# Optimization experiments

Measured on AMD Instinct MI355X. Metric: run time of the kernel, lower is better.

The kernel has to match this reference:

```python
import jax, jax.numpy as jnp
import numpy as np

WIN = 9
EPS = 1e-05


def _box3d(x, win=WIN):
    """Sum over a win^3 box (zero-padded), equivalent to conv3d with a ones kernel.
    Implemented as three separable 1D convolutions (exact same math, O(win)/voxel)."""
    pad = win // 2
    for axis in range(3):  # spatial axes D, H, W
        kshape = [1, 1, 1, 1, 1]
        kshape[2 + axis] = win
        kern = jnp.ones(kshape, x.dtype)
        pads = [(0, 0)] * 3
        pads[axis] = (pad, pad)
        dn = jax.lax.conv_dimension_numbers(x.shape, kern.shape, ('NCDHW', 'OIDHW', 'NCDHW'))
        x = jax.lax.conv_general_dilated(x, kern, window_strides=(1, 1, 1),
                                         padding=pads, dimension_numbers=dn)
    return x


def setup_inputs() -> dict:
    key = jax.random.key(0)
    k1, k2 = jax.random.split(key)
    shape = (1, 1, 160, 192, 224)  # [N, C, D, H, W] brain-MRI-scale volume
    I = jax.random.normal(k1, shape, dtype=jnp.float32)
    J = jax.random.normal(k2, shape, dtype=jnp.float32)
    return {"I": I, "J": J}


def reference(I, J):
    win_size = WIN ** 3
    I2 = I * I
    J2 = J * J
    IJ = I * J
    I_sum = _box3d(I)
    J_sum = _box3d(J)
    I2_sum = _box3d(I2)
    J2_sum = _box3d(J2)
    IJ_sum = _box3d(IJ)
    u_I = I_sum / win_size
    u_J = J_sum / win_size
    cross = IJ_sum - u_J * I_sum - u_I * J_sum + u_I * u_J * win_size
    I_var = I2_sum - 2 * u_I * I_sum + u_I * u_I * win_size
    J_var = J2_sum - 2 * u_J * J_sum + u_J * u_J * win_size
    cc = cross * cross / (I_var * J_var + EPS)
    return -1.0 * jnp.mean(cc)
```

## Files before the change

### kernel.cpp

```cpp
#include <hip/hip_runtime.h>


#define DD 160
#define HH 192
#define WW 224
#define W4 56
#define SLICE (HH * WW)
#define S4 (SLICE / 4)
#define NVOX (DD * SLICE)
#define TW 32
#define TH 8
#define DCH 28
#define ITERS (DCH + 8)
#define NTHR 256
#define SW_RS 36
#define SW_CS (16 * SW_RS)
#define SH_SZ (TH * TW * 5)
#define EPS 1e-5f
#define INV_WSUM (1.0f / 729.0f)

__device__ __forceinline__ void bar_lds_only() {
    __asm__ volatile("" ::: "memory");
    __builtin_amdgcn_s_waitcnt(0xC07F);
    __builtin_amdgcn_s_barrier();
    __asm__ volatile("" ::: "memory");
}

__global__ __launch_bounds__(NTHR, 4) void ncc_fused(const float* __restrict__ I,
                                                     const float* __restrict__ J,
                                                     float* __restrict__ out) {
    __shared__ float SW0[5 * SW_CS], SW1[5 * SW_CS];
    __shared__ float SH0[SH_SZ], SH1[SH_SZ];
    __shared__ float wred[NTHR / 64];

    const int tid = threadIdx.x;
    const int tx = tid & 31, ty = tid >> 5;
    const int wlo = blockIdx.x * TW;
    const int hlo = blockIdx.y * TH;
    const int dlo = blockIdx.z * DCH;

    const int wid = tid - 128;
    const int wr = wid >> 3, wc = wid & 7;
    const int gh = hlo - 4 + wr;
    const bool hok = (gh >= 0) && (gh < HH);
    const int gf0 = (wlo >> 2) - 1 + wc;

    const int hcol = tid & 31, hch = tid >> 5;

    const float4* Iv = (const float4*)I;
    const float4* Jv = (const float4*)J;

    float pfa[12], pfb[12];

    auto w_load = [&](int z) {
        const bool zok = (z >= 0) && (z < DD) && hok;
        const int rowb = z * S4 + gh * W4;
        #pragma unroll
        for (int k = 0; k < 3; ++k) {
            const int f = gf0 + k;
            float4 a = make_float4(0.f, 0.f, 0.f, 0.f);
            float4 b = make_float4(0.f, 0.f, 0.f, 0.f);
            if (zok && f >= 0 && f < W4) { a = Iv[rowb + f]; b = Jv[rowb + f]; }
            pfa[4*k] = a.x; pfa[4*k+1] = a.y; pfa[4*k+2] = a.z; pfa[4*k+3] = a.w;
            pfb[4*k] = b.x; pfb[4*k+1] = b.y; pfb[4*k+2] = b.z; pfb[4*k+3] = b.w;
        }
    };

    auto w_compute = [&](float* dst) {
        float* wp = dst + wr * SW_RS + 4 * wc;
        #pragma unroll
        for (int ch = 0; ch < 5; ++ch) {
            float v[12];
            #pragma unroll
            for (int k = 0; k < 12; ++k)
                v[k] = (ch == 0) ? pfa[k]
                     : (ch == 1) ? pfb[k]
                     : (ch == 2) ? pfa[k] * pfa[k]
                     : (ch == 3) ? pfb[k] * pfb[k]
                     :             pfa[k] * pfb[k];
            float s = v[0];
            #pragma unroll
            for (int k = 1; k < 9; ++k) s += v[k];
            float4 o;
            o.x = s;
            s += v[9]  - v[0]; o.y = s;
            s += v[10] - v[1]; o.z = s;
            s += v[11] - v[2]; o.w = s;
            *(float4*)(wp + ch * SW_CS) = o;
        }
    };

    auto h_phase = [&](const float* swSrc, float* shDst) {
        const float* p = swSrc + hch * SW_CS + hcol;
        float v[16];
        #pragma unroll
        for (int r = 0; r < 16; r += 2) {
            const float* pr = p + r * SW_RS;
            v[r]     = pr[0];
            v[r + 1] = pr[SW_RS];
        }
        float s = v[0];
        #pragma unroll
        for (int r = 1; r < 9; ++r) s += v[r];
        float* o = shDst + hcol * 5 + hch;
        float prev = s;
        o[0] = s;
        #pragma unroll
        for (int r = 1; r < TH; ++r) {
            prev += v[r + 8] - v[r - 1];
            o[r * (TW * 5)] = prev;
        }
    };

    float q0[9], q1[9], q2[9], q3[9], q4[9];
    #pragma unroll
    for (int k = 0; k < 9; ++k) { q0[k]=0.f; q1[k]=0.f; q2[k]=0.f; q3[k]=0.f; q4[k]=0.f; }
    float r0=0.f, r1=0.f, r2=0.f, r3=0.f, r4=0.f;
    float acc = 0.f;

    const int z0 = dlo - 4;
    if (tid >= 128) {
        w_load(z0);
        if (z0 >= 0) w_compute(SW0);
        w_load(z0 + 1);
    }
    bar_lds_only();

    if (tid < 160 && z0 >= 0) h_phase(SW0, SH0);
    if (tid >= 128) {
        const int z1 = z0 + 1;
        if (z1 >= 0 && z1 < DD) w_compute(SW1);
        w_load(z0 + 2);
    }

    #pragma unroll 1
    for (int g = 0; g < 4; ++g) {
        #pragma unroll
        for (int ph = 0; ph < 9; ++ph) {
            const int j = 9 * g + ph;
            const int z = dlo - 4 + j;
            bar_lds_only();

            const bool val = (z >= 0) && (z < DD);
            float* shR = (j & 1) ? SH1 : SH0;
            float w0=0.f, w1=0.f, w2=0.f, w3=0.f, w4=0.f;
            if (val) {
                const float* pF = shR + (ty * TW + tx) * 5;
                w0 = pF[0]; w1 = pF[1]; w2 = pF[2]; w3 = pF[3]; w4 = pF[4];
            }

            if ((g < 3 || ph < 8) && tid < 160) {
                const int zh = z + 1;
                if (zh >= 0 && zh < DD)
                    h_phase((j & 1) ? SW0 : SW1, (j & 1) ? SH0 : SH1);
            }

            if ((g < 3 || ph < 7) && tid >= 128) {
                const int zw = z + 2;
                if (zw >= 0 && zw < DD) w_compute((j & 1) ? SW1 : SW0);
                w_load(z + 3);
            }

            r0 += w0 - q0[ph]; q0[ph] = w0;
            r1 += w1 - q1[ph]; q1[ph] = w1;
            r2 += w2 - q2[ph]; q2[ph] = w2;
            r3 += w3 - q3[ph]; q3[ph] = w3;
            r4 += w4 - q4[ph]; q4[ph] = w4;

            if (j >= 8 && (dlo + j - 8) < DD) {
                float cross = r4 - r0 * r1 * INV_WSUM;
                float iv    = r2 - r0 * r0 * INV_WSUM;
                float jv    = r3 - r1 * r1 * INV_WSUM;
                acc += cross * cross * __builtin_amdgcn_rcpf(iv * jv + EPS);
            }
        }
    }

    #pragma unroll
    for (int off = 32; off > 0; off >>= 1) acc += __shfl_down(acc, off, 64);
    if ((tid & 63) == 0) wred[tid >> 6] = acc;
    __syncthreads();
    if (tid == 0) {
        float t = 0.f;
        #pragma unroll
        for (int k = 0; k < NTHR / 64; ++k) t += wred[k];
        atomicAdd(out, t * (-1.0f / (float)NVOX));
    }
}

extern "C" void kernel_launch(void* const* d_in, const int* in_sizes, int n_in,
                              void* d_out, int out_size, void* d_ws, size_t ws_size,
                              hipStream_t stream) {
    const float* I = (const float*)d_in[0];
    const float* J = (const float*)d_in[1];
    float* out = (float*)d_out;

    hipMemsetAsync(d_out, 0, sizeof(float), stream);

    dim3 blk(NTHR, 1, 1);
    dim3 grd(WW / TW, HH / TH, (DD + DCH - 1) / DCH);
    ncc_fused<<<grd, blk, 0, stream>>>(I, J, out);
}
```

Before: 126.0 us.

## Double-buffer global prefetch registers to load two depth slices ahead

Adds a second set of prefetch registers so global loads for slice z+4 are issued while slice z+2 is being processed, deepening the load pipeline from one slice ahead to two. The inner loop is unrolled to 18 phases so the register-buffer choice and the LDS-buffer parity stay compile-time constant, and the ring index becomes ph%9. This aims to hide more global-memory latency, at the cost of 24 extra VGPRs per thread and a larger unrolled body, which could lower occupancy under the 4-blocks-per-SM launch bound.

```diff
diff --git a/kernel.cpp b/kernel.cpp
--- a/kernel.cpp
+++ b/kernel.cpp
@@ -50,45 +50,51 @@
     const float4* Iv = (const float4*)I;
     const float4* Jv = (const float4*)J;
 
-    float pfa[12], pfb[12];
-
-    auto w_load = [&](int z) {
-        const bool zok = (z >= 0) && (z < DD) && hok;
-        const int rowb = z * S4 + gh * W4;
-        #pragma unroll
-        for (int k = 0; k < 3; ++k) {
-            const int f = gf0 + k;
-            float4 a = make_float4(0.f, 0.f, 0.f, 0.f);
-            float4 b = make_float4(0.f, 0.f, 0.f, 0.f);
-            if (zok && f >= 0 && f < W4) { a = Iv[rowb + f]; b = Jv[rowb + f]; }
-            pfa[4*k] = a.x; pfa[4*k+1] = a.y; pfa[4*k+2] = a.z; pfa[4*k+3] = a.w;
-            pfb[4*k] = b.x; pfb[4*k+1] = b.y; pfb[4*k+2] = b.z; pfb[4*k+3] = b.w;
-        }
-    };
-
-    auto w_compute = [&](float* dst) {
-        float* wp = dst + wr * SW_RS + 4 * wc;
-        #pragma unroll
-        for (int ch = 0; ch < 5; ++ch) {
-            float v[12];
-            #pragma unroll
-            for (int k = 0; k < 12; ++k)
-                v[k] = (ch == 0) ? pfa[k]
-                     : (ch == 1) ? pfb[k]
-                     : (ch == 2) ? pfa[k] * pfa[k]
-                     : (ch == 3) ? pfb[k] * pfb[k]
-                     :             pfa[k] * pfb[k];
-            float s = v[0];
-            #pragma unroll
-            for (int k = 1; k < 9; ++k) s += v[k];
-            float4 o;
-            o.x = s;
-            s += v[9]  - v[0]; o.y = s;
-            s += v[10] - v[1]; o.z = s;
-            s += v[11] - v[2]; o.w = s;
-            *(float4*)(wp + ch * SW_CS) = o;
-        }
-    };
+    float pfa0[12], pfb0[12], pfa1[12], pfb1[12];
+
+#define DEF_WLOAD(NAME, PA, PB)                                               \
+    auto NAME = [&](int z) {                                                  \
+        const bool zok = (z >= 0) && (z < DD) && hok;                         \
+        const int rowb = z * S4 + gh * W4;                                    \
+        _Pragma("unroll")                                                     \
+        for (int k = 0; k < 3; ++k) {                                         \
+            const int f = gf0 + k;                                            \
+            float4 a = make_float4(0.f, 0.f, 0.f, 0.f);                       \
+            float4 b = make_float4(0.f, 0.f, 0.f, 0.f);                       \
+            if (zok && f >= 0 && f < W4) { a = Iv[rowb + f]; b = Jv[rowb + f]; } \
+            PA[4*k] = a.x; PA[4*k+1] = a.y; PA[4*k+2] = a.z; PA[4*k+3] = a.w; \
+            PB[4*k] = b.x; PB[4*k+1] = b.y; PB[4*k+2] = b.z; PB[4*k+3] = b.w; \
+        }                                                                     \
+    }
+    DEF_WLOAD(w_load0, pfa0, pfb0);
+    DEF_WLOAD(w_load1, pfa1, pfb1);
+
+#define DEF_WCOMP(NAME, PA, PB)                                               \
+    auto NAME = [&](float* dst) {                                             \
+        float* wp = dst + wr * SW_RS + 4 * wc;                                \
+        _Pragma("unroll")                                                     \
+        for (int ch = 0; ch < 5; ++ch) {                                      \
+            float v[12];                                                      \
+            _Pragma("unroll")                                                 \
+            for (int k = 0; k < 12; ++k)                                      \
+                v[k] = (ch == 0) ? PA[k]                                      \
+                     : (ch == 1) ? PB[k]                                      \
+                     : (ch == 2) ? PA[k] * PA[k]                              \
+                     : (ch == 3) ? PB[k] * PB[k]                              \
+                     :             PA[k] * PB[k];                             \
+            float s = v[0];                                                   \
+            _Pragma("unroll")                                                 \
+            for (int k = 1; k < 9; ++k) s += v[k];                            \
+            float4 o;                                                         \
+            o.x = s;                                                          \
+            s += v[9]  - v[0]; o.y = s;                                       \
+            s += v[10] - v[1]; o.z = s;                                       \
+            s += v[11] - v[2]; o.w = s;                                       \
+            *(float4*)(wp + ch * SW_CS) = o;                                  \
+        }                                                                     \
+    }
+    DEF_WCOMP(w_comp0, pfa0, pfb0);
+    DEF_WCOMP(w_comp1, pfa1, pfb1);
 
     auto h_phase = [&](const float* swSrc, float* shDst) {
         const float* p = swSrc + hch * SW_CS + hcol;
@@ -120,54 +126,61 @@
 
     const int z0 = dlo - 4;
     if (tid >= 128) {
-        w_load(z0);
-        if (z0 >= 0) w_compute(SW0);
-        w_load(z0 + 1);
+        w_load0(z0);
+        if (z0 >= 0) w_comp0(SW0);
+        w_load0(z0 + 1);
     }
     bar_lds_only();
 
     if (tid < 160 && z0 >= 0) h_phase(SW0, SH0);
     if (tid >= 128) {
         const int z1 = z0 + 1;
-        if (z1 >= 0 && z1 < DD) w_compute(SW1);
-        w_load(z0 + 2);
+        if (z1 >= 0 && z1 < DD) w_comp0(SW1);
+        w_load0(z0 + 2);
+        w_load1(z0 + 3);
     }
 
     #pragma unroll 1
-    for (int g = 0; g < 4; ++g) {
-        #pragma unroll
-        for (int ph = 0; ph < 9; ++ph) {
-            const int j = 9 * g + ph;
+    for (int g = 0; g < 2; ++g) {
+        #pragma unroll
+        for (int ph = 0; ph < 18; ++ph) {
+            const int j = 18 * g + ph;
             const int z = dlo - 4 + j;
             bar_lds_only();
 
             const bool val = (z >= 0) && (z < DD);
-            float* shR = (j & 1) ? SH1 : SH0;
+            float* shR = (ph & 1) ? SH1 : SH0;
             float w0=0.f, w1=0.f, w2=0.f, w3=0.f, w4=0.f;
             if (val) {
                 const float* pF = shR + (ty * TW + tx) * 5;
                 w0 = pF[0]; w1 = pF[1]; w2 = pF[2]; w3 = pF[3]; w4 = pF[4];
             }
 
-            if ((g < 3 || ph < 8) && tid < 160) {
+            if ((g == 0 || ph < 17) && tid < 160) {
                 const int zh = z + 1;
                 if (zh >= 0 && zh < DD)
-                    h_phase((j & 1) ? SW0 : SW1, (j & 1) ? SH0 : SH1);
-            }
-
-            if ((g < 3 || ph < 7) && tid >= 128) {
+                    h_phase((ph & 1) ? SW0 : SW1, (ph & 1) ? SH0 : SH1);
+            }
+
+            if ((g == 0 || ph < 16) && tid >= 128) {
                 const int zw = z + 2;
-                if (zw >= 0 && zw < DD) w_compute((j & 1) ? SW1 : SW0);
-                w_load(z + 3);
-            }
-
-            r0 += w0 - q0[ph]; q0[ph] = w0;
-            r1 += w1 - q1[ph]; q1[ph] = w1;
-            r2 += w2 - q2[ph]; q2[ph] = w2;
-            r3 += w3 - q3[ph]; q3[ph] = w3;
-            r4 += w4 - q4[ph]; q4[ph] = w4;
-
-            if (j >= 8 && (dlo + j - 8) < DD) {
+                if ((ph & 1) == 0) {
+                    if (zw >= 0 && zw < DD) w_comp0((ph & 1) ? SW1 : SW0);
+                    w_load0(z + 4);
+                } else {
+                    if (zw >= 0 && zw < DD) w_comp1((ph & 1) ? SW1 : SW0);
+                    w_load1(z + 4);
+                }
+            }
+
+            const int rq = ph % 9;
+            r0 += w0 - q0[rq]; q0[rq] = w0;
+            r1 += w1 - q1[rq]; q1[rq] = w1;
+            r2 += w2 - q2[rq]; q2[rq] = w2;
+            r3 += w3 - q3[rq]; q3[rq] = w3;
+            r4 += w4 - q4[rq]; q4[rq] = w4;
+
+            if ((g > 0 || ph >= 8) && (dlo + j - 8) < DD) {
                 float cross = r4 - r0 * r1 * INV_WSUM;
                 float iv    = r2 - r0 * r0 * INV_WSUM;
                 float jv    = r3 - r1 * r1 * INV_WSUM;
```

Result: slower. 234.2 us (+85.8%).
